# Optimization experiments

Measured on AMD Instinct MI355X. Metric: run time of the kernel, lower is better.

## Reference

```python
import jax, jax.numpy as jnp
import numpy as np

N = 400000      # active voxels
INC = 64
OUTC = 64
GRID = 128      # voxel grid extent per axis
K = 27          # 3x3x3 kernel offsets
EPS = 1e-5      # BatchNorm eps


def setup_inputs() -> dict:
    rng = np.random.default_rng(0)
    # unique sorted voxel keys in a GRID^3 volume (hash = linearized coord)
    flat = np.sort(rng.choice(GRID ** 3, size=N, replace=False)).astype(np.int64)
    cx = flat // (GRID * GRID)
    cy = (flat // GRID) % GRID
    cz = flat % GRID
    offsets = [(dx, dy, dz) for dx in (-1, 0, 1) for dy in (-1, 0, 1) for dz in (-1, 0, 1)]
    in_idx = np.zeros((K, N), np.int32)
    out_idx = np.zeros((K, N), np.int32)
    mask = np.zeros((K, N), np.float32)
    # kernel map: for each offset, hash-lookup which input voxels have an output voxel at coord+offset
    for k, (dx, dy, dz) in enumerate(offsets):
        nx, ny, nz = cx + dx, cy + dy, cz + dz
        valid = (nx >= 0) & (nx < GRID) & (ny >= 0) & (ny < GRID) & (nz >= 0) & (nz < GRID)
        nkey = nx * GRID * GRID + ny * GRID + nz
        pos = np.searchsorted(flat, nkey)
        pos_c = np.clip(pos, 0, N - 1)
        found = valid & (flat[pos_c] == nkey)
        src = np.nonzero(found)[0]
        dst = pos_c[src]
        p = src.size
        in_idx[k, :p] = src
        out_idx[k, :p] = dst
        mask[k, :p] = 1.0
    key = jax.random.key(0)
    k1, k2 = jax.random.split(key, 2)
    feats = jax.random.normal(k1, (N, INC), jnp.float32)
    W = jax.random.normal(k2, (K, INC, OUTC), jnp.float32) * (1.0 / np.sqrt(INC * K))
    gamma = jnp.ones((OUTC,), jnp.float32)
    beta = jnp.zeros((OUTC,), jnp.float32)
    return {
        "feats": feats,
        "W": W,
        "gamma": gamma,
        "beta": beta,
        "pair_mask": jnp.asarray(mask),
        "in_idx": jnp.asarray(in_idx),
        "out_idx": jnp.asarray(out_idx),
    }


def reference(feats, W, gamma, beta, pair_mask, in_idx, out_idx):
    # sparse transposed conv3d as gather -> matmul -> scatter-add per kernel offset
    n, outc = feats.shape[0], W.shape[2]
    out = jnp.zeros((n, outc), feats.dtype)
    for k in range(W.shape[0]):  # fixed small loop over 27 kernel offsets
        g = feats[in_idx[k]] * pair_mask[k][:, None]   # [N, INC], padded pairs zeroed
        out = out.at[out_idx[k]].add(g @ W[k])         # scatter into output voxels
    # BatchNorm (training-mode batch stats over voxels) + ReLU
    mean = out.mean(axis=0)
    var = out.var(axis=0)
    y = (out - mean) * jax.lax.rsqrt(var + EPS) * gamma + beta
    return jax.nn.relu(y)
```

## Files before the change

### kernel.cpp

```cpp
#include <hip/hip_runtime.h>
#include <stdint.h>

typedef unsigned short u16;
typedef unsigned int u32;

#define NV 400000
#define KOFF 27
#define EPS_BN 1e-5f

#define INV_ELEMS (KOFF * NV)
#define INV_BYTES (INV_ELEMS * 4)
#define FEATSBF_OFF INV_BYTES
#define WT_OFF (FEATSBF_OFF + NV * 64 * 2)
#define STATS_OFF (WT_OFF + KOFF * 64 * 64 * 2)

#define CVT_BLOCKS 25000
#define BUILD_BLOCKS 42188
#define WT_BLOCKS 432
#define PREP_BLOCKS (CVT_BLOCKS + BUILD_BLOCKS + WT_BLOCKS)

using short8 = __attribute__((ext_vector_type(8))) short;
using floatx16 = __attribute__((ext_vector_type(16))) float;

__device__ __forceinline__ u16 f2bf(float f) {
  u32 u = __float_as_uint(f);
  u += 0x7FFFu + ((u >> 16) & 1u);
  return (u16)(u >> 16);
}

__global__ void k_prep(const float* __restrict__ feats, u16* __restrict__ featsBf,
                       const int* __restrict__ in_idx, const int* __restrict__ out_idx,
                       const float* __restrict__ mask, int* __restrict__ inv,
                       const float* __restrict__ W, u16* __restrict__ Wt) {
  const int b = blockIdx.x;
  const int tid = threadIdx.x;
  if (b < CVT_BLOCKS) {
    int i = b * 256 + tid;
    float4 v = ((const float4*)feats)[i];
    ushort4 o;
    o.x = f2bf(v.x); o.y = f2bf(v.y); o.z = f2bf(v.z); o.w = f2bf(v.w);
    ((ushort4*)featsBf)[i] = o;
  } else if (b < CVT_BLOCKS + BUILD_BLOCKS) {
    int t = (b - CVT_BLOCKS) * 256 + tid;
    if (t < INV_ELEMS && mask[t] != 0.0f) {
      int k = t / NV;
      inv[k * NV + out_idx[t]] = in_idx[t];
    }
  } else {
    int t = (b - CVT_BLOCKS - BUILD_BLOCKS) * 256 + tid;
    if (t < KOFF * 64 * 64) {
      int k = t >> 12, rem = t & 4095, c = rem >> 6, o = rem & 63;
      Wt[(k << 12) + (o << 6) + c] = f2bf(W[t]);
    }
  }
}

__global__ void __launch_bounds__(256)
k_main(const u16* __restrict__ feats, const int* __restrict__ inv,
       const u16* __restrict__ Wt, float* __restrict__ out, float* __restrict__ stats) {
  __shared__ u16 Wsm[2][64][72];
  __shared__ float redS[4][64];
  __shared__ float redQ[4][64];

  const int t = threadIdx.x;
  const int lane = t & 63;
  const int wave = t >> 6;
  const int lo = lane & 31;
  const int hi = lane >> 5;
  const int rbase = blockIdx.x * 256 + wave * 64;
  const int row0 = rbase + lo;
  const int row1 = rbase + 32 + lo;
  const bool v0 = row0 < NV;
  const bool v1 = row1 < NV;

  const floatx16 z16 = {0.f, 0.f, 0.f, 0.f, 0.f, 0.f, 0.f, 0.f,
                        0.f, 0.f, 0.f, 0.f, 0.f, 0.f, 0.f, 0.f};
  floatx16 acc00 = z16, acc01 = z16, acc10 = z16, acc11 = z16;

  const int wr0 = t >> 3;
  const int wc0 = (t & 7) * 8;

#define GATHER(A0, A1, s0, s1)                                        \
  {                                                                   \
    const short8 z8 = {0, 0, 0, 0, 0, 0, 0, 0};                       \
    A0[0] = z8; A0[1] = z8; A0[2] = z8; A0[3] = z8;                   \
    A1[0] = z8; A1[1] = z8; A1[2] = z8; A1[3] = z8;                   \
    if ((s0) >= 0) {                                                  \
      const u16* p = feats + (s0) * 64 + hi * 8;                      \
      A0[0] = *(const short8*)(p);                                    \
      A0[1] = *(const short8*)(p + 16);                               \
      A0[2] = *(const short8*)(p + 32);                               \
      A0[3] = *(const short8*)(p + 48);                               \
    }                                                                 \
    if ((s1) >= 0) {                                                  \
      const u16* p = feats + (s1) * 64 + hi * 8;                      \
      A1[0] = *(const short8*)(p);                                    \
      A1[1] = *(const short8*)(p + 16);                               \
      A1[2] = *(const short8*)(p + 32);                               \
      A1[3] = *(const short8*)(p + 48);                               \
    }                                                                 \
  }

#define DOMFMA(BUF, A0, A1)                                                     \
  _Pragma("unroll")                                                             \
  for (int kk = 0; kk < 4; ++kk) {                                              \
    short8 b0 = *(const short8*)&Wsm[BUF][lo][kk * 16 + hi * 8];                \
    short8 b1 = *(const short8*)&Wsm[BUF][32 + lo][kk * 16 + hi * 8];           \
    acc00 = __builtin_amdgcn_mfma_f32_32x32x16_bf16(A0[kk], b0, acc00, 0, 0, 0);\
    acc01 = __builtin_amdgcn_mfma_f32_32x32x16_bf16(A0[kk], b1, acc01, 0, 0, 0);\
    acc10 = __builtin_amdgcn_mfma_f32_32x32x16_bf16(A1[kk], b0, acc10, 0, 0, 0);\
    acc11 = __builtin_amdgcn_mfma_f32_32x32x16_bf16(A1[kk], b1, acc11, 0, 0, 0);\
  }

  uint4 wEa = *(const uint4*)(Wt + t * 8);
  uint4 wEb = *(const uint4*)(Wt + (t + 256) * 8);
  uint4 wOa = wEa, wOb = wEb;
  int sC0 = v0 ? inv[row0] : -1;
  int sC1 = v1 ? inv[row1] : -1;
  int sO0 = v0 ? inv[NV + row0] : -1;
  int sO1 = v1 ? inv[NV + row1] : -1;
  int sE0 = -1, sE1 = -1;

  short8 Ac0[4], Ac1[4], An0[4], An1[4];
  GATHER(Ac0, Ac1, sC0, sC1);

  for (int k = 0; k < KOFF; k += 2) {
    *(uint4*)&Wsm[0][wr0][wc0] = wEa;
    *(uint4*)&Wsm[0][wr0 + 32][wc0] = wEb;
    if (k + 1 < KOFF) {
      const u16* wk = Wt + ((k + 1) << 12);
      wOa = *(const uint4*)(wk + t * 8);
      wOb = *(const uint4*)(wk + (t + 256) * 8);
    }
    if (k + 2 < KOFF) {
      const int* ik = inv + (k + 2) * NV;
      sE0 = v0 ? ik[row0] : -1;
      sE1 = v1 ? ik[row1] : -1;
    }
    if (k + 1 < KOFF) GATHER(An0, An1, sO0, sO1);
    __syncthreads();
    DOMFMA(0, Ac0, Ac1);
    if (k + 1 >= KOFF) break;
    *(uint4*)&Wsm[1][wr0][wc0] = wOa;
    *(uint4*)&Wsm[1][wr0 + 32][wc0] = wOb;
    if (k + 2 < KOFF) {
      const u16* wk = Wt + ((k + 2) << 12);
      wEa = *(const uint4*)(wk + t * 8);
      wEb = *(const uint4*)(wk + (t + 256) * 8);
    }
    if (k + 3 < KOFF) {
      const int* ik = inv + (k + 3) * NV;
      sO0 = v0 ? ik[row0] : -1;
      sO1 = v1 ? ik[row1] : -1;
    }
    if (k + 2 < KOFF) GATHER(Ac0, Ac1, sE0, sE1);
    __syncthreads();
    DOMFMA(1, An0, An1);
  }
#undef GATHER
#undef DOMFMA

  float s0 = 0.f, q0 = 0.f, s1 = 0.f, q1 = 0.f;
#pragma unroll
  for (int r = 0; r < 16; ++r) {
    s0 += acc00[r] + acc10[r];
    q0 += acc00[r] * acc00[r] + acc10[r] * acc10[r];
    s1 += acc01[r] + acc11[r];
    q1 += acc01[r] * acc01[r] + acc11[r] * acc11[r];
  }
  s0 += __shfl_xor(s0, 32, 64); q0 += __shfl_xor(q0, 32, 64);
  s1 += __shfl_xor(s1, 32, 64); q1 += __shfl_xor(q1, 32, 64);
  if (lane < 32) {
    redS[wave][lo] = s0; redQ[wave][lo] = q0;
    redS[wave][32 + lo] = s1; redQ[wave][32 + lo] = q1;
  }

#pragma unroll
  for (int r = 0; r < 16; ++r) {
    int rl = (r & 3) + ((r >> 2) * 8) + hi * 4;
    int ra = rbase + rl;
    int rb = rbase + 32 + rl;
    if (ra < NV) { out[ra * 64 + lo] = acc00[r]; out[ra * 64 + 32 + lo] = acc01[r]; }
    if (rb < NV) { out[rb * 64 + lo] = acc10[r]; out[rb * 64 + 32 + lo] = acc11[r]; }
  }

  __syncthreads();
  if (t < 64) {
    float s = redS[0][t] + redS[1][t] + redS[2][t] + redS[3][t];
    float q = redQ[0][t] + redQ[1][t] + redQ[2][t] + redQ[3][t];
    atomicAdd(&stats[t], s);
    atomicAdd(&stats[64 + t], q);
  }
}

__global__ void k_apply(float* __restrict__ out, const float* __restrict__ stats,
                        const float* __restrict__ gamma, const float* __restrict__ beta) {
  __shared__ float sc[64], sh[64];
  const int t = threadIdx.x;
  if (t < 64) {
    float inv_n = 1.0f / (float)NV;
    float mean = stats[t] * inv_n;
    float var = stats[64 + t] * inv_n - mean * mean;
    float scale = gamma[t] * rsqrtf(var + EPS_BN);
    sc[t] = scale;
    sh[t] = beta[t] - mean * scale;
  }
  __syncthreads();
  int i = blockIdx.x * 256 + t;
  if (i >= NV * 64 / 4) return;
  int c0 = (i & 15) * 4;
  float4 v = ((const float4*)out)[i];
  float* pv = (float*)&v;
#pragma unroll
  for (int j = 0; j < 4; ++j) {
    float y = pv[j] * sc[c0 + j] + sh[c0 + j];
    pv[j] = y > 0.f ? y : 0.f;
  }
  ((float4*)out)[i] = v;
}

extern "C" void kernel_launch(void* const* d_in, const int* in_sizes, int n_in,
                              void* d_out, int out_size, void* d_ws, size_t ws_size,
                              hipStream_t stream) {
  const float* feats = (const float*)d_in[0];
  const float* W     = (const float*)d_in[1];
  const float* gamma = (const float*)d_in[2];
  const float* beta  = (const float*)d_in[3];
  const float* mask  = (const float*)d_in[4];
  const int* in_idx  = (const int*)d_in[5];
  const int* out_idx = (const int*)d_in[6];
  float* out = (float*)d_out;

  char* ws = (char*)d_ws;
  int* inv = (int*)ws;
  u16* featsBf = (u16*)(ws + FEATSBF_OFF);
  u16* Wt = (u16*)(ws + WT_OFF);
  float* stats = (float*)(ws + STATS_OFF);

  hipMemsetAsync(inv, 0xFF, INV_BYTES, stream);
  hipMemsetAsync(stats, 0, 128 * sizeof(float), stream);
  k_prep<<<PREP_BLOCKS, 256, 0, stream>>>(feats, featsBf, in_idx, out_idx, mask, inv, W, Wt);
  k_main<<<(NV + 255) / 256, 256, 0, stream>>>(featsBf, inv, Wt, out, stats);
  k_apply<<<NV * 64 / 4 / 256, 256, 0, stream>>>(out, stats, gamma, beta);
}
```

Baseline: 404.4 us.

## Read weights directly from global memory instead of staging in LDS

```diff
diff --git a/kernel.cpp b/kernel.cpp
--- a/kernel.cpp
+++ b/kernel.cpp
@@ -55,10 +55,9 @@
   }
 }
 
-__global__ void __launch_bounds__(256)
+__global__ void __launch_bounds__(256, 3)
 k_main(const u16* __restrict__ feats, const int* __restrict__ inv,
        const u16* __restrict__ Wt, float* __restrict__ out, float* __restrict__ stats) {
-  __shared__ u16 Wsm[2][64][72];
   __shared__ float redS[4][64];
   __shared__ float redQ[4][64];
 
@@ -77,8 +76,7 @@
                         0.f, 0.f, 0.f, 0.f, 0.f, 0.f, 0.f, 0.f};
   floatx16 acc00 = z16, acc01 = z16, acc10 = z16, acc11 = z16;
 
-  const int wr0 = t >> 3;
-  const int wc0 = (t & 7) * 8;
+  const u16* wbase = Wt + lo * 64 + hi * 8;
 
 #define GATHER(A0, A1, s0, s1)                                        \
   {                                                                   \
@@ -101,61 +99,43 @@
     }                                                                 \
   }
 
-#define DOMFMA(BUF, A0, A1)                                                     \
-  _Pragma("unroll")                                                             \
-  for (int kk = 0; kk < 4; ++kk) {                                              \
-    short8 b0 = *(const short8*)&Wsm[BUF][lo][kk * 16 + hi * 8];                \
-    short8 b1 = *(const short8*)&Wsm[BUF][32 + lo][kk * 16 + hi * 8];           \
-    acc00 = __builtin_amdgcn_mfma_f32_32x32x16_bf16(A0[kk], b0, acc00, 0, 0, 0);\
-    acc01 = __builtin_amdgcn_mfma_f32_32x32x16_bf16(A0[kk], b1, acc01, 0, 0, 0);\
-    acc10 = __builtin_amdgcn_mfma_f32_32x32x16_bf16(A1[kk], b0, acc10, 0, 0, 0);\
-    acc11 = __builtin_amdgcn_mfma_f32_32x32x16_bf16(A1[kk], b1, acc11, 0, 0, 0);\
-  }
-
-  uint4 wEa = *(const uint4*)(Wt + t * 8);
-  uint4 wEb = *(const uint4*)(Wt + (t + 256) * 8);
-  uint4 wOa = wEa, wOb = wEb;
+#define DOMFMA(KIDX, A0, A1)                                                    \
+  {                                                                             \
+    const u16* wk = wbase + ((KIDX) << 12);                                     \
+    _Pragma("unroll")                                                           \
+    for (int kk = 0; kk < 4; ++kk) {                                            \
+      short8 b0 = *(const short8*)(wk + kk * 16);                               \
+      short8 b1 = *(const short8*)(wk + 2048 + kk * 16);                        \
+      acc00 = __builtin_amdgcn_mfma_f32_32x32x16_bf16(A0[kk], b0, acc00, 0, 0, 0);\
+      acc01 = __builtin_amdgcn_mfma_f32_32x32x16_bf16(A0[kk], b1, acc01, 0, 0, 0);\
+      acc10 = __builtin_amdgcn_mfma_f32_32x32x16_bf16(A1[kk], b0, acc10, 0, 0, 0);\
+      acc11 = __builtin_amdgcn_mfma_f32_32x32x16_bf16(A1[kk], b1, acc11, 0, 0, 0);\
+    }                                                                           \
+  }
+
   int sC0 = v0 ? inv[row0] : -1;
   int sC1 = v1 ? inv[row1] : -1;
-  int sO0 = v0 ? inv[NV + row0] : -1;
-  int sO1 = v1 ? inv[NV + row1] : -1;
-  int sE0 = -1, sE1 = -1;
-
   short8 Ac0[4], Ac1[4], An0[4], An1[4];
   GATHER(Ac0, Ac1, sC0, sC1);
+  int sN0 = v0 ? inv[NV + row0] : -1;
+  int sN1 = v1 ? inv[NV + row1] : -1;
 
   for (int k = 0; k < KOFF; k += 2) {
-    *(uint4*)&Wsm[0][wr0][wc0] = wEa;
-    *(uint4*)&Wsm[0][wr0 + 32][wc0] = wEb;
-    if (k + 1 < KOFF) {
-      const u16* wk = Wt + ((k + 1) << 12);
-      wOa = *(const uint4*)(wk + t * 8);
-      wOb = *(const uint4*)(wk + (t + 256) * 8);
-    }
+    if (k + 1 < KOFF) GATHER(An0, An1, sN0, sN1);
     if (k + 2 < KOFF) {
       const int* ik = inv + (k + 2) * NV;
-      sE0 = v0 ? ik[row0] : -1;
-      sE1 = v1 ? ik[row1] : -1;
-    }
-    if (k + 1 < KOFF) GATHER(An0, An1, sO0, sO1);
-    __syncthreads();
-    DOMFMA(0, Ac0, Ac1);
+      sN0 = v0 ? ik[row0] : -1;
+      sN1 = v1 ? ik[row1] : -1;
+    }
+    DOMFMA(k, Ac0, Ac1);
     if (k + 1 >= KOFF) break;
-    *(uint4*)&Wsm[1][wr0][wc0] = wOa;
-    *(uint4*)&Wsm[1][wr0 + 32][wc0] = wOb;
-    if (k + 2 < KOFF) {
-      const u16* wk = Wt + ((k + 2) << 12);
-      wEa = *(const uint4*)(wk + t * 8);
-      wEb = *(const uint4*)(wk + (t + 256) * 8);
-    }
+    if (k + 2 < KOFF) GATHER(Ac0, Ac1, sN0, sN1);
     if (k + 3 < KOFF) {
       const int* ik = inv + (k + 3) * NV;
-      sO0 = v0 ? ik[row0] : -1;
-      sO1 = v1 ? ik[row1] : -1;
-    }
-    if (k + 2 < KOFF) GATHER(Ac0, Ac1, sE0, sE1);
-    __syncthreads();
-    DOMFMA(1, An0, An1);
+      sN0 = v0 ? ik[row0] : -1;
+      sN1 = v1 ? ik[row1] : -1;
+    }
+    DOMFMA(k + 1, An0, An1);
   }
 #undef GATHER
 #undef DOMFMA
```

After: 531.9 us. 31.5% more time.
